# Performance work log

Measured on AMD Instinct MI355X. Metric: run time of the kernel, lower is better.

Reference implementation:

```python
import jax, jax.numpy as jnp
import numpy as np

EPS = 1e-5
N_LAYERS_TOTAL = 4  # n_layers + 1 convs


def setup_inputs() -> dict:
    key = jax.random.key(0)
    ks = jax.random.split(key, 6)
    B, N, C = 16, 2048, 128
    x = jax.random.normal(ks[0], (B, N, C), dtype=jnp.float32)
    adj = jax.random.uniform(ks[1], (B, N, N), dtype=jnp.float32)
    # per-layer params: weight [L,Cin,Cout], bias [L,Cout], bn gamma/beta [L,C]
    W = jax.random.normal(ks[2], (N_LAYERS_TOTAL, C, C), dtype=jnp.float32) * (1.0 / np.sqrt(C))
    b = jnp.zeros((N_LAYERS_TOTAL, C), dtype=jnp.float32)
    gamma = jnp.ones((N_LAYERS_TOTAL, C), dtype=jnp.float32)
    beta = jnp.zeros((N_LAYERS_TOTAL, C), dtype=jnp.float32)
    return {"x": x, "adj": adj, "W": W, "b": b, "gamma": gamma, "beta": beta}


def reference(x, adj, W, b, gamma, beta):
    # Stacked dense GCNConv -> ReLU -> BatchNorm1d (training mode).
    h = x
    for i in range(N_LAYERS_TOTAL):
        # GCNConv (dense, normalize=False): adj @ (h @ W) + b
        h = jnp.einsum('bnm,bmc->bnc', adj, h @ W[i]) + b[i]  # [B,N,C]
        h = jax.nn.relu(h)
        # BatchNorm over flattened (B*N) per channel, biased variance
        mu = jnp.mean(h, axis=(0, 1))
        var = jnp.mean(jnp.square(h - mu), axis=(0, 1))
        h = gamma[i] * (h - mu) * jax.lax.rsqrt(var + EPS) + beta[i]
    return h
```

## Files before the change

kernel.cpp:

```cpp
#include <hip/hip_runtime.h>
#include <stdint.h>
#include <stddef.h>

#define BATCH 16
#define NROW 2048
#define CH 128
#define NLAYER 4
#define NN_TOT (BATCH * NROW)
#define EPSV 1e-5f
#define KS 64

typedef short short8 __attribute__((ext_vector_type(8)));
typedef float f32x4 __attribute__((ext_vector_type(4)));

static __device__ __forceinline__ unsigned short f2bf(float f) {
  union { float f; unsigned int i; } v;
  v.f = f;
  unsigned int u = v.i;
  return (unsigned short)((u + 0x7FFFu + ((u >> 16) & 1u)) >> 16);
}

__global__ void init_kernel(const float* __restrict__ W,
                            unsigned short* __restrict__ Wt4,
                            float* __restrict__ gsum, float* __restrict__ gsumsq) {
  const int l = blockIdx.x;
  const int t = threadIdx.x;
  const float* Wl = W + (size_t)l * CH * CH;
  unsigned short* Wo = Wt4 + (size_t)l * CH * CH;
  for (int idx = t; idx < CH * CH; idx += 256) {
    int o = idx >> 7, c = idx & 127;
    Wo[idx] = f2bf(Wl[c * CH + o]);
  }
  if (l == 0) {
    for (int i = t; i < NLAYER * CH; i += 256) { gsum[i] = 0.0f; gsumsq[i] = 0.0f; }
  }
}

template <int FIRST>
__global__ __launch_bounds__(256) void gemm1_kernel(
    const float* __restrict__ X,
    const unsigned short* __restrict__ Wt,
    const float* __restrict__ gp, const float* __restrict__ bp,
    const float* __restrict__ gsumP, const float* __restrict__ gsumsqP,
    unsigned short* __restrict__ Yt) {
  __shared__ unsigned short As[64 * 128];
  __shared__ unsigned short Bs[128 * 128];
  __shared__ __align__(16) float ss[CH];
  __shared__ __align__(16) float tt[CH];
  const int tid = threadIdx.x;
  const int m0 = blockIdx.x * 64;

  if (!FIRST) {
    if (tid < CH) {
      const float inv = 1.0f / (float)NN_TOT;
      float mu = gsumP[tid] * inv;
      float var = gsumsqP[tid] * inv - mu * mu;
      float s_ = gp[tid] * rsqrtf(var + EPSV);
      ss[tid] = s_;
      tt[tid] = bp[tid] - mu * s_;
    }
    __syncthreads();
  }

#pragma unroll
  for (int j = 0; j < 4; ++j) {
    int c = tid + 256 * j;
    int r = c >> 4, slot = c & 15;
    int kc = slot ^ (r & 15);
    const float* p = X + (size_t)(m0 + r) * CH + kc * 8;
    f32x4 a = *(const f32x4*)p;
    f32x4 b = *(const f32x4*)(p + 4);
    if (!FIRST) {
      f32x4 sa = *(const f32x4*)(ss + kc * 8);
      f32x4 sb = *(const f32x4*)(ss + kc * 8 + 4);
      f32x4 ta = *(const f32x4*)(tt + kc * 8);
      f32x4 tb = *(const f32x4*)(tt + kc * 8 + 4);
      a = sa * a + ta;
      b = sb * b + tb;
    }
    short8 v;
    v[0] = (short)f2bf(a[0]); v[1] = (short)f2bf(a[1]);
    v[2] = (short)f2bf(a[2]); v[3] = (short)f2bf(a[3]);
    v[4] = (short)f2bf(b[0]); v[5] = (short)f2bf(b[1]);
    v[6] = (short)f2bf(b[2]); v[7] = (short)f2bf(b[3]);
    *(short8*)(As + c * 8) = v;
  }
#pragma unroll
  for (int j = 0; j < 8; ++j) {
    int c = tid + 256 * j;
    int r = c >> 4, slot = c & 15;
    int kc = slot ^ (r & 15);
    *(short8*)(Bs + c * 8) = *(const short8*)(Wt + (size_t)r * CH + kc * 8);
  }
  __syncthreads();

  const int l = tid & 63, w = tid >> 6;
  const int mq = (w >> 1) * 32, oq = (w & 1) * 64;
  const int lr = l & 15, lq = l >> 4;
  f32x4 acc[2][4] = {};

#pragma unroll
  for (int kt = 0; kt < 4; ++kt) {
    const int kc0 = kt * 4 + lq;
    const int slotK = kc0 ^ lr;
    short8 a[2], b[4];
#pragma unroll
    for (int mi = 0; mi < 2; ++mi)
      a[mi] = *(const short8*)(As + (mq + mi * 16 + lr) * 128 + slotK * 8);
#pragma unroll
    for (int ni = 0; ni < 4; ++ni)
      b[ni] = *(const short8*)(Bs + (oq + ni * 16 + lr) * 128 + slotK * 8);
#pragma unroll
    for (int mi = 0; mi < 2; ++mi)
#pragma unroll
      for (int ni = 0; ni < 4; ++ni)
        acc[mi][ni] = __builtin_amdgcn_mfma_f32_16x16x32_bf16(a[mi], b[ni], acc[mi][ni], 0, 0, 0);
  }

  const int bat = m0 >> 11;
  const int mb = m0 & 2047;
  unsigned short* YtB = Yt + (size_t)bat * CH * NROW;
#pragma unroll
  for (int ni = 0; ni < 4; ++ni) {
    const int o = oq + ni * 16 + lr;
    unsigned short* row = YtB + (size_t)o * NROW;
#pragma unroll
    for (int mi = 0; mi < 2; ++mi) {
      const int m = mb + mq + mi * 16 + lq * 4;
      f32x4 v = acc[mi][ni];
      unsigned short p0 = f2bf(v[0]), p1 = f2bf(v[1]);
      unsigned short p2 = f2bf(v[2]), p3 = f2bf(v[3]);
      unsigned long long packed = (unsigned long long)p0 | ((unsigned long long)p1 << 16) |
                                  ((unsigned long long)p2 << 32) | ((unsigned long long)p3 << 48);
      *(unsigned long long*)(row + m) = packed;
    }
  }
}

struct Pf {
  short8 b0, b1;
  f32x4 f0, f1, f2, f3;
};

template <int CVT>
__global__ __launch_bounds__(256) void gemm2_kernel(
    const float* __restrict__ adjF,
    const unsigned short* __restrict__ adjH,
    unsigned short* __restrict__ adjO,
    const unsigned short* __restrict__ Yt,
    const float* __restrict__ bias,
    float* __restrict__ R,
    float* __restrict__ gsumL, float* __restrict__ gsumsqL) {
  __shared__ unsigned short Bs[2][64 * KS];
  __shared__ float redS[2][CH];
  __shared__ float redQ[2][CH];

  const int tid = threadIdx.x;
  const int bat = blockIdx.x >> 5;
  const int n0 = (blockIdx.x & 31) * 64;
  const unsigned short* YtB = Yt + (size_t)bat * CH * NROW;

  const int s8 = tid & 7;
  const int r8 = tid >> 3;
  const int swz8 = (s8 ^ (r8 & 7)) * 8;
  const size_t bO0 = (size_t)bat * NROW * NROW + (size_t)(n0 + r8) * NROW + s8 * 8;
  const size_t bO1 = bO0 + (size_t)32 * NROW;
  const int lB0 = r8 * KS + swz8;
  const int lB1 = lB0 + 32 * KS;

  const int l = tid & 63, w = tid >> 6;
  const int cq = (w >> 1) * 64;
  const int nh = (w & 1) * 32;
  const int lr = l & 15, lq = l >> 4;
  const int rsw = lr & 7;

  const unsigned short* aBase = YtB + (size_t)(cq + lr) * NROW + lq * 8;

  f32x4 acc[4][2] = {};

  auto LOADB = [&](Pf& p, int kt) {
    const int k0 = kt * KS;
    if constexpr (CVT) {
      const float* q0 = adjF + bO0 + k0;
      const float* q1 = adjF + bO1 + k0;
      p.f0 = *(const f32x4*)q0; p.f1 = *(const f32x4*)(q0 + 4);
      p.f2 = *(const f32x4*)q1; p.f3 = *(const f32x4*)(q1 + 4);
    } else {
      p.b0 = *(const short8*)(adjH + bO0 + k0);
      p.b1 = *(const short8*)(adjH + bO1 + k0);
    }
  };

  auto WRITEB = [&](Pf& p, int buf, int kt) {
    unsigned short* Bp = Bs[buf];
    if constexpr (CVT) {
      short8 q0, q1;
      q0[0] = (short)f2bf(p.f0[0]); q0[1] = (short)f2bf(p.f0[1]);
      q0[2] = (short)f2bf(p.f0[2]); q0[3] = (short)f2bf(p.f0[3]);
      q0[4] = (short)f2bf(p.f1[0]); q0[5] = (short)f2bf(p.f1[1]);
      q0[6] = (short)f2bf(p.f1[2]); q0[7] = (short)f2bf(p.f1[3]);
      q1[0] = (short)f2bf(p.f2[0]); q1[1] = (short)f2bf(p.f2[1]);
      q1[2] = (short)f2bf(p.f2[2]); q1[3] = (short)f2bf(p.f2[3]);
      q1[4] = (short)f2bf(p.f3[0]); q1[5] = (short)f2bf(p.f3[1]);
      q1[6] = (short)f2bf(p.f3[2]); q1[7] = (short)f2bf(p.f3[3]);
      *(short8*)(Bp + lB0) = q0;
      *(short8*)(Bp + lB1) = q1;
      const int k0 = kt * KS;
      *(short8*)(adjO + bO0 + k0) = q0;
      *(short8*)(adjO + bO1 + k0) = q1;
    } else {
      *(short8*)(Bp + lB0) = p.b0;
      *(short8*)(Bp + lB1) = p.b1;
    }
  };

  auto LOADA = [&](short8* ar, int kt) {
    const int k0 = kt * KS;
#pragma unroll
    for (int mi = 0; mi < 4; ++mi)
#pragma unroll
      for (int ks = 0; ks < 2; ++ks)
        ar[mi * 2 + ks] = *(const short8*)(aBase + (size_t)mi * 16 * NROW + k0 + ks * 32);
  };

  auto COMPUTE = [&](int buf, const short8* ar) {
    const unsigned short* Bp = Bs[buf];
#pragma unroll
    for (int ks = 0; ks < 2; ++ks) {
      const int sl = ((ks * 4 + lq) ^ rsw) * 8;
      short8 b0 = *(const short8*)(Bp + (nh + 0 + lr) * KS + sl);
      short8 b1 = *(const short8*)(Bp + (nh + 16 + lr) * KS + sl);
#pragma unroll
      for (int mi = 0; mi < 4; ++mi) {
        acc[mi][0] = __builtin_amdgcn_mfma_f32_16x16x32_bf16(ar[mi * 2 + ks], b0, acc[mi][0], 0, 0, 0);
        acc[mi][1] = __builtin_amdgcn_mfma_f32_16x16x32_bf16(ar[mi * 2 + ks], b1, acc[mi][1], 0, 0, 0);
      }
    }
  };

#define BAR() do { asm volatile("s_waitcnt lgkmcnt(0)"); __builtin_amdgcn_s_barrier(); } while (0)

  Pf s0, s1;
  short8 arX[8], arY[8];
  LOADB(s0, 0);
  LOADA(arX, 0);
  WRITEB(s0, 0, 0);
  LOADB(s0, 1);
  LOADB(s1, 2);
  BAR();

#pragma unroll 1
  for (int kt2 = 0; kt2 < 14; ++kt2) {
    const int kt = kt2 * 2;
    LOADA(arY, kt + 1);
    WRITEB(s0, 1, kt + 1);
    LOADB(s0, kt + 3);
    COMPUTE(0, arX);
    BAR();
    LOADA(arX, kt + 2);
    WRITEB(s1, 0, kt + 2);
    LOADB(s1, kt + 4);
    COMPUTE(1, arY);
    BAR();
  }
  LOADA(arY, 29);
  WRITEB(s0, 1, 29);
  LOADB(s0, 31);
  COMPUTE(0, arX);
  BAR();
  LOADA(arX, 30);
  WRITEB(s1, 0, 30);
  COMPUTE(1, arY);
  BAR();
  LOADA(arY, 31);
  WRITEB(s0, 1, 31);
  COMPUTE(0, arX);
  BAR();
  COMPUTE(1, arY);
#undef BAR

  float* RB = R + (size_t)bat * NROW * CH;
  f32x4 sumv[4] = {};
  f32x4 sumq[4] = {};
#pragma unroll
  for (int mi = 0; mi < 4; ++mi) {
    const int c0 = cq + mi * 16 + lq * 4;
    f32x4 bia = *(const f32x4*)(bias + c0);
#pragma unroll
    for (int ni = 0; ni < 2; ++ni) {
      const int n = n0 + nh + ni * 16 + lr;
      f32x4 v = acc[mi][ni] + bia;
      v[0] = fmaxf(v[0], 0.0f);
      v[1] = fmaxf(v[1], 0.0f);
      v[2] = fmaxf(v[2], 0.0f);
      v[3] = fmaxf(v[3], 0.0f);
      sumv[mi] += v;
      sumq[mi] += v * v;
      *(f32x4*)(RB + (size_t)n * CH + c0) = v;
    }
  }
#pragma unroll
  for (int mi = 0; mi < 4; ++mi) {
#pragma unroll
    for (int d = 1; d < 16; d <<= 1) {
      sumv[mi][0] += __shfl_xor(sumv[mi][0], d);
      sumv[mi][1] += __shfl_xor(sumv[mi][1], d);
      sumv[mi][2] += __shfl_xor(sumv[mi][2], d);
      sumv[mi][3] += __shfl_xor(sumv[mi][3], d);
      sumq[mi][0] += __shfl_xor(sumq[mi][0], d);
      sumq[mi][1] += __shfl_xor(sumq[mi][1], d);
      sumq[mi][2] += __shfl_xor(sumq[mi][2], d);
      sumq[mi][3] += __shfl_xor(sumq[mi][3], d);
    }
  }
  const int nqi = w & 1;
  if (lr == 0) {
#pragma unroll
    for (int mi = 0; mi < 4; ++mi) {
      const int c0 = cq + mi * 16 + lq * 4;
      redS[nqi][c0 + 0] = sumv[mi][0];
      redS[nqi][c0 + 1] = sumv[mi][1];
      redS[nqi][c0 + 2] = sumv[mi][2];
      redS[nqi][c0 + 3] = sumv[mi][3];
      redQ[nqi][c0 + 0] = sumq[mi][0];
      redQ[nqi][c0 + 1] = sumq[mi][1];
      redQ[nqi][c0 + 2] = sumq[mi][2];
      redQ[nqi][c0 + 3] = sumq[mi][3];
    }
  }
  __syncthreads();
  if (tid < CH) {
    atomicAdd(gsumL + tid, redS[0][tid] + redS[1][tid]);
  } else {
    const int c = tid - CH;
    atomicAdd(gsumsqL + c, redQ[0][c] + redQ[1][c]);
  }
}

__global__ __launch_bounds__(256) void out_kernel(
    float* __restrict__ out,
    const float* __restrict__ g3, const float* __restrict__ b3,
    const float* __restrict__ gsum3, const float* __restrict__ gsumsq3) {
  __shared__ __align__(16) float ss[CH];
  __shared__ __align__(16) float tt[CH];
  if (threadIdx.x < CH) {
    const float inv = 1.0f / (float)NN_TOT;
    float mu = gsum3[threadIdx.x] * inv;
    float var = gsumsq3[threadIdx.x] * inv - mu * mu;
    float s_ = g3[threadIdx.x] * rsqrtf(var + EPSV);
    ss[threadIdx.x] = s_;
    tt[threadIdx.x] = b3[threadIdx.x] - mu * s_;
  }
  __syncthreads();
  const int total = NN_TOT * CH / 4;
  for (int idx = blockIdx.x * blockDim.x + threadIdx.x; idx < total;
       idx += gridDim.x * blockDim.x) {
    f32x4 v = *(f32x4*)(out + (size_t)idx * 4);
    const int c0 = (idx & 31) * 4;
    f32x4 s = *(const f32x4*)(ss + c0);
    f32x4 t = *(const f32x4*)(tt + c0);
    v = s * v + t;
    *(f32x4*)(out + (size_t)idx * 4) = v;
  }
}

extern "C" void kernel_launch(void* const* d_in, const int* in_sizes, int n_in,
                              void* d_out, int out_size, void* d_ws, size_t ws_size,
                              hipStream_t stream) {
  (void)in_sizes; (void)n_in; (void)out_size; (void)ws_size;
  const float* x     = (const float*)d_in[0];
  const float* adj   = (const float*)d_in[1];
  const float* W     = (const float*)d_in[2];
  const float* bvec  = (const float*)d_in[3];
  const float* gamma = (const float*)d_in[4];
  const float* beta  = (const float*)d_in[5];

  float* R = (float*)d_out;

  char* ws = (char*)d_ws;
  unsigned short* adjb = (unsigned short*)(ws);
  unsigned short* Yt   = (unsigned short*)(ws + 134217728);
  unsigned short* Wt4  = (unsigned short*)(ws + 142606336);
  float* gsum   = (float*)(ws + 142606336 + 131072);
  float* gsumsq = (float*)(ws + 142606336 + 131072 + 2048);

  init_kernel<<<4, 256, 0, stream>>>(W, Wt4, gsum, gsumsq);

  for (int i = 0; i < NLAYER; ++i) {
    if (i == 0) {
      gemm1_kernel<1><<<512, 256, 0, stream>>>(
          x, Wt4, nullptr, nullptr, nullptr, nullptr, Yt);
      gemm2_kernel<1><<<512, 256, 0, stream>>>(
          adj, nullptr, adjb, Yt, bvec, R, gsum, gsumsq);
    } else {
      gemm1_kernel<0><<<512, 256, 0, stream>>>(
          R, Wt4 + (size_t)i * CH * CH,
          gamma + (size_t)(i - 1) * CH, beta + (size_t)(i - 1) * CH,
          gsum + (size_t)(i - 1) * CH, gsumsq + (size_t)(i - 1) * CH, Yt);
      gemm2_kernel<0><<<512, 256, 0, stream>>>(
          nullptr, adjb, nullptr, Yt, bvec + (size_t)i * CH, R,
          gsum + (size_t)i * CH, gsumsq + (size_t)i * CH);
    }
  }
  out_kernel<<<512, 256, 0, stream>>>(R, gamma + 3 * CH, beta + 3 * CH,
                                      gsum + 3 * CH, gsumsq + 3 * CH);
}
```

Baseline: 684.0 us.

## Stage Yt operand through double-buffered LDS in gemm2 instead of direct global loads

In gemm2, the Yt (A) operand is no longer loaded straight from global memory into registers per wave. The whole block now loads it cooperatively into a swizzled, double-buffered LDS tile alongside the adjacency tile, and the waves read it from LDS. Compute is reordered to run before each stage's shared-memory write, with prefetch kept in registers. This removes redundant global loads of Yt across waves that share the same channel rows, at the cost of extra LDS capacity (about 32KB more per block, lowering occupancy) and more LDS traffic. The init kernel also moves the stat zeroing into a separate block.

Result: faster. 587.9 us (-14.1%).

```diff
diff --git a/kernel.cpp b/kernel.cpp
--- a/kernel.cpp
+++ b/kernel.cpp
@@ -25,13 +25,14 @@
                             float* __restrict__ gsum, float* __restrict__ gsumsq) {
   const int l = blockIdx.x;
   const int t = threadIdx.x;
-  const float* Wl = W + (size_t)l * CH * CH;
-  unsigned short* Wo = Wt4 + (size_t)l * CH * CH;
-  for (int idx = t; idx < CH * CH; idx += 256) {
-    int o = idx >> 7, c = idx & 127;
-    Wo[idx] = f2bf(Wl[c * CH + o]);
-  }
-  if (l == 0) {
+  if (l < NLAYER) {
+    const float* Wl = W + (size_t)l * CH * CH;
+    unsigned short* Wo = Wt4 + (size_t)l * CH * CH;
+    for (int idx = t; idx < CH * CH; idx += 256) {
+      int o = idx >> 7, c = idx & 127;
+      Wo[idx] = f2bf(Wl[c * CH + o]);
+    }
+  } else {
     for (int i = t; i < NLAYER * CH; i += 256) { gsum[i] = 0.0f; gsumsq[i] = 0.0f; }
   }
 }
@@ -138,6 +139,7 @@
 }
 
 struct Pf {
+  short8 a0, a1, a2, a3;
   short8 b0, b1;
   f32x4 f0, f1, f2, f3;
 };
@@ -151,6 +153,7 @@
     const float* __restrict__ bias,
     float* __restrict__ R,
     float* __restrict__ gsumL, float* __restrict__ gsumsqL) {
+  __shared__ unsigned short As[2][CH * KS];
   __shared__ unsigned short Bs[2][64 * KS];
   __shared__ float redS[2][CH];
   __shared__ float redQ[2][CH];
@@ -163,6 +166,16 @@
   const int s8 = tid & 7;
   const int r8 = tid >> 3;
   const int swz8 = (s8 ^ (r8 & 7)) * 8;
+
+  const unsigned short* gA0 = YtB + (size_t)r8 * NROW + s8 * 8;
+  const unsigned short* gA1 = gA0 + (size_t)32 * NROW;
+  const unsigned short* gA2 = gA0 + (size_t)64 * NROW;
+  const unsigned short* gA3 = gA0 + (size_t)96 * NROW;
+  const int lA0 = r8 * KS + swz8;
+  const int lA1 = lA0 + 32 * KS;
+  const int lA2 = lA0 + 64 * KS;
+  const int lA3 = lA0 + 96 * KS;
+
   const size_t bO0 = (size_t)bat * NROW * NROW + (size_t)(n0 + r8) * NROW + s8 * 8;
   const size_t bO1 = bO0 + (size_t)32 * NROW;
   const int lB0 = r8 * KS + swz8;
@@ -174,12 +187,14 @@
   const int lr = l & 15, lq = l >> 4;
   const int rsw = lr & 7;
 
-  const unsigned short* aBase = YtB + (size_t)(cq + lr) * NROW + lq * 8;
-
   f32x4 acc[4][2] = {};
 
-  auto LOADB = [&](Pf& p, int kt) {
+  auto LOADS = [&](Pf& p, int kt) {
     const int k0 = kt * KS;
+    p.a0 = *(const short8*)(gA0 + k0);
+    p.a1 = *(const short8*)(gA1 + k0);
+    p.a2 = *(const short8*)(gA2 + k0);
+    p.a3 = *(const short8*)(gA3 + k0);
     if constexpr (CVT) {
       const float* q0 = adjF + bO0 + k0;
       const float* q1 = adjF + bO1 + k0;
@@ -191,7 +206,12 @@
     }
   };
 
-  auto WRITEB = [&](Pf& p, int buf, int kt) {
+  auto WRITES = [&](Pf& p, int buf, int kt) {
+    unsigned short* Ap = As[buf];
+    *(short8*)(Ap + lA0) = p.a0;
+    *(short8*)(Ap + lA1) = p.a1;
+    *(short8*)(Ap + lA2) = p.a2;
+    *(short8*)(Ap + lA3) = p.a3;
     unsigned short* Bp = Bs[buf];
     if constexpr (CVT) {
       short8 q0, q1;
@@ -214,69 +234,61 @@
     }
   };
 
-  auto LOADA = [&](short8* ar, int kt) {
-    const int k0 = kt * KS;
-#pragma unroll
-    for (int mi = 0; mi < 4; ++mi)
-#pragma unroll
-      for (int ks = 0; ks < 2; ++ks)
-        ar[mi * 2 + ks] = *(const short8*)(aBase + (size_t)mi * 16 * NROW + k0 + ks * 32);
-  };
-
-  auto COMPUTE = [&](int buf, const short8* ar) {
+  auto COMPUTE = [&](int buf) {
+    const unsigned short* Ap = As[buf];
     const unsigned short* Bp = Bs[buf];
 #pragma unroll
     for (int ks = 0; ks < 2; ++ks) {
       const int sl = ((ks * 4 + lq) ^ rsw) * 8;
-      short8 b0 = *(const short8*)(Bp + (nh + 0 + lr) * KS + sl);
+      short8 a0 = *(const short8*)(Ap + (cq +  0 + lr) * KS + sl);
+      short8 a1 = *(const short8*)(Ap + (cq + 16 + lr) * KS + sl);
+      short8 a2 = *(const short8*)(Ap + (cq + 32 + lr) * KS + sl);
+      short8 a3 = *(const short8*)(Ap + (cq + 48 + lr) * KS + sl);
+      short8 b0 = *(const short8*)(Bp + (nh +  0 + lr) * KS + sl);
       short8 b1 = *(const short8*)(Bp + (nh + 16 + lr) * KS + sl);
-#pragma unroll
-      for (int mi = 0; mi < 4; ++mi) {
-        acc[mi][0] = __builtin_amdgcn_mfma_f32_16x16x32_bf16(ar[mi * 2 + ks], b0, acc[mi][0], 0, 0, 0);
-        acc[mi][1] = __builtin_amdgcn_mfma_f32_16x16x32_bf16(ar[mi * 2 + ks], b1, acc[mi][1], 0, 0, 0);
-      }
+      acc[0][0] = __builtin_amdgcn_mfma_f32_16x16x32_bf16(a0, b0, acc[0][0], 0, 0, 0);
+      acc[0][1] = __builtin_amdgcn_mfma_f32_16x16x32_bf16(a0, b1, acc[0][1], 0, 0, 0);
+      acc[1][0] = __builtin_amdgcn_mfma_f32_16x16x32_bf16(a1, b0, acc[1][0], 0, 0, 0);
+      acc[1][1] = __builtin_amdgcn_mfma_f32_16x16x32_bf16(a1, b1, acc[1][1], 0, 0, 0);
+      acc[2][0] = __builtin_amdgcn_mfma_f32_16x16x32_bf16(a2, b0, acc[2][0], 0, 0, 0);
+      acc[2][1] = __builtin_amdgcn_mfma_f32_16x16x32_bf16(a2, b1, acc[2][1], 0, 0, 0);
+      acc[3][0] = __builtin_amdgcn_mfma_f32_16x16x32_bf16(a3, b0, acc[3][0], 0, 0, 0);
+      acc[3][1] = __builtin_amdgcn_mfma_f32_16x16x32_bf16(a3, b1, acc[3][1], 0, 0, 0);
     }
   };
 
 #define BAR() do { asm volatile("s_waitcnt lgkmcnt(0)"); __builtin_amdgcn_s_barrier(); } while (0)
 
   Pf s0, s1;
-  short8 arX[8], arY[8];
-  LOADB(s0, 0);
-  LOADA(arX, 0);
-  WRITEB(s0, 0, 0);
-  LOADB(s0, 1);
-  LOADB(s1, 2);
+  LOADS(s0, 0);
+  WRITES(s0, 0, 0);
+  LOADS(s0, 1);
+  LOADS(s1, 2);
   BAR();
 
 #pragma unroll 1
   for (int kt2 = 0; kt2 < 14; ++kt2) {
     const int kt = kt2 * 2;
-    LOADA(arY, kt + 1);
-    WRITEB(s0, 1, kt + 1);
-    LOADB(s0, kt + 3);
-    COMPUTE(0, arX);
+    COMPUTE(0);
+    WRITES(s0, 1, kt + 1);
+    LOADS(s0, kt + 3);
     BAR();
-    LOADA(arX, kt + 2);
-    WRITEB(s1, 0, kt + 2);
-    LOADB(s1, kt + 4);
-    COMPUTE(1, arY);
+    COMPUTE(1);
+    WRITES(s1, 0, kt + 2);
+    LOADS(s1, kt + 4);
     BAR();
   }
-  LOADA(arY, 29);
-  WRITEB(s0, 1, 29);
-  LOADB(s0, 31);
-  COMPUTE(0, arX);
+  COMPUTE(0);
+  WRITES(s0, 1, 29);
+  LOADS(s0, 31);
   BAR();
-  LOADA(arX, 30);
-  WRITEB(s1, 0, 30);
-  COMPUTE(1, arY);
+  COMPUTE(1);
+  WRITES(s1, 0, 30);
   BAR();
-  LOADA(arY, 31);
-  WRITEB(s0, 1, 31);
-  COMPUTE(0, arX);
+  COMPUTE(0);
+  WRITES(s0, 1, 31);
   BAR();
-  COMPUTE(1, arY);
+  COMPUTE(1);
 #undef BAR
 
   float* RB = R + (size_t)bat * NROW * CH;
@@ -384,7 +396,7 @@
   float* gsum   = (float*)(ws + 142606336 + 131072);
   float* gsumsq = (float*)(ws + 142606336 + 131072 + 2048);
 
-  init_kernel<<<4, 256, 0, stream>>>(W, Wt4, gsum, gsumsq);
+  init_kernel<<<NLAYER + 1, 256, 0, stream>>>(W, Wt4, gsum, gsumsq);
 
   for (int i = 0; i < NLAYER; ++i) {
     if (i == 0) {
```
